# Performance work log

Hardware: AMD Instinct MI355X
Metric: run time of the kernel (lower is better)

## Reference

```python
import jax, jax.numpy as jnp
import numpy as np

HEADS = 8
FEATURE = 512
COMPUTE = 256
SEQ = 512
BATCH = 64


def setup_inputs() -> dict:
    key = jax.random.key(0)
    ks = jax.random.split(key, 10)
    d1 = jax.random.normal(ks[0], (BATCH, FEATURE), dtype=jnp.float32)
    d2 = jax.random.normal(ks[1], (SEQ, BATCH, FEATURE), dtype=jnp.float32)
    # linear1: Linear(FEATURE -> COMPUTE) + ReLU
    w1 = jax.random.normal(ks[2], (FEATURE, COMPUTE), dtype=jnp.float32) * (1.0 / np.sqrt(FEATURE))
    b1 = jnp.zeros((COMPUTE,), dtype=jnp.float32)
    # per-head score params, stacked: ws[i] is [2C, C], ps[i] is [C, 1]
    W = jax.random.normal(ks[3], (HEADS, 2 * COMPUTE, COMPUTE), dtype=jnp.float32)
    P = jax.random.normal(ks[4], (HEADS, COMPUTE), dtype=jnp.float32)
    # value projection weight_v: [FEATURE, COMPUTE]
    wv = jax.random.normal(ks[5], (FEATURE, COMPUTE), dtype=jnp.float32)
    # cc: Linear(COMPUTE*HEADS -> 128) + ReLU
    wcc = jax.random.normal(ks[6], (COMPUTE * HEADS, 128), dtype=jnp.float32) * (1.0 / np.sqrt(COMPUTE * HEADS))
    bcc = jnp.zeros((128,), dtype=jnp.float32)
    return {"d1": d1, "d2": d2, "w1": w1, "b1": b1, "W": W, "P": P,
            "wv": wv, "wcc": wcc, "bcc": bcc, "d2_size": SEQ}


def reference(d1, d2, w1, b1, W, P, wv, wcc, bcc, d2_size):
    S, B, F = d2.shape
    # linear1 on flattened d2 rows -> [S*B, C]
    d3 = jax.nn.relu(d2.reshape(-1, F) @ w1 + b1)
    # linear1 on d1, tiled S times along batch axis -> [S*B, C]
    d4 = jax.nn.relu(d1 @ w1 + b1)            # [B, C]
    d4 = jnp.tile(d4, (S, 1))                  # [S*B, C]
    d5 = jnp.concatenate([d3, d4], axis=1).reshape(S, B, -1)  # [S, B, 2C]
    # value path: tanh(d2 @ weight_v) -> [B, S, C]
    tv = jnp.tanh(jnp.einsum('sbf,fc->sbc', d2, wv)).transpose(1, 0, 2)
    # all heads batched: us = tanh(d5 @ W_h) -> [H, S, B, C]
    us = jnp.tanh(jnp.einsum('sbd,hdc->hsbc', d5, W))
    atts = jnp.einsum('hsbc,hc->hbs', us, P)   # [H, B, S]
    scores = jax.nn.softmax(atts, axis=-1)     # softmax over sequence
    vs = jnp.einsum('hbs,bsc->hbc', scores, tv)  # weighted sum over S -> [H, B, C]
    # torch.cat(vs, dim=1): head-major concat -> [B, H*C]
    vs = vs.transpose(1, 0, 2).reshape(B, -1)
    return jax.nn.relu(vs @ wcc + bcc)         # [B, 128]
```

## Files before the change

### kernel.cpp

```cpp
#include <hip/hip_runtime.h>
#include <cstddef>
#include <cstdint>

#define HH 8
#define FF 512
#define CC 256
#define SS 512
#define BB 64
#define SB (SS*BB)
#define PAD 34

typedef __attribute__((ext_vector_type(4))) float f32x4;
typedef __attribute__((ext_vector_type(8))) short bf16x8;

__device__ __forceinline__ float fast_tanh(float x) {
    float e = __expf(2.0f * x);
    return 1.0f - 2.0f / (e + 1.0f);
}
__device__ __forceinline__ float relu_f(float x) { return fmaxf(x, 0.0f); }

__device__ __forceinline__ unsigned short f2bf(float x) {
    unsigned u = __float_as_uint(x);
    unsigned r = u + 0x7FFFu + ((u >> 16) & 1u);
    return (unsigned short)(r >> 16);
}
__device__ __forceinline__ float bf2f(unsigned short h) {
    return __uint_as_float(((unsigned)h) << 16);
}

__global__ __launch_bounds__(256) void p_prep(
    const float* __restrict__ w1, const float* __restrict__ wv,
    const float* __restrict__ W, const float* __restrict__ d1,
    const float* __restrict__ b1,
    unsigned short* __restrict__ w1t_hi, unsigned short* __restrict__ w1t_lo,
    unsigned short* __restrict__ wvt_hi, unsigned short* __restrict__ wvt_lo,
    unsigned short* __restrict__ Wt_hi, unsigned short* __restrict__ Wt_lo,
    float* __restrict__ d4, float* __restrict__ atts)
{
    __shared__ float T[64][65];
    __shared__ float As[16][68];
    __shared__ float Bs[16][68];
    const int tid = threadIdx.x;
    const int bid = blockIdx.x;
    if (bid >= 196) {
        f32x4 z = {0.0f, 0.0f, 0.0f, 0.0f};
        *(f32x4*)(atts + (size_t)(bid - 196) * 1024 + tid * 4) = z;
        return;
    }
    if (bid < 192) {
        const float* src;
        unsigned short *dhi, *dlo;
        int K, kt, nt;
        if (bid < 64) {
            int m = bid >> 5;
            int t = bid & 31;
            kt = t >> 2; nt = t & 3; K = FF;
            src = m ? wv : w1;
            dhi = m ? wvt_hi : w1t_hi;
            dlo = m ? wvt_lo : w1t_lo;
        } else {
            int t = bid - 64;
            int h = t >> 4; int tt = t & 15;
            kt = tt >> 2; nt = tt & 3; K = CC;
            src = W + (size_t)h * 2 * CC * CC;
            dhi = Wt_hi + (size_t)h * CC * CC;
            dlo = Wt_lo + (size_t)h * CC * CC;
        }
        const int k0 = kt * 64, n0 = nt * 64;
        #pragma unroll
        for (int jj = 0; jj < 4; ++jj) {
            int i = (tid >> 4) + jj * 16;
            int j = (tid & 15) * 4;
            float4 v = *(const float4*)(src + (size_t)(k0 + i) * CC + n0 + j);
            T[i][j] = v.x; T[i][j+1] = v.y; T[i][j+2] = v.z; T[i][j+3] = v.w;
        }
        __syncthreads();
        #pragma unroll
        for (int jj = 0; jj < 4; ++jj) {
            int n = (tid >> 4) + jj * 16;
            int kq = (tid & 15) * 4;
            unsigned short hv[4], lv[4];
            #pragma unroll
            for (int q = 0; q < 4; ++q) {
                float x = T[kq + q][n];
                unsigned short hx = f2bf(x);
                hv[q] = hx; lv[q] = f2bf(x - bf2f(hx));
            }
            size_t o = (size_t)(n0 + n) * K + k0 + kq;
            *(ushort4*)(dhi + o) = *(ushort4*)hv;
            *(ushort4*)(dlo + o) = *(ushort4*)lv;
        }
    } else {
        const int n0 = (bid - 192) * 64;
        const int tx = tid & 15, ty = tid >> 4;
        const int lm = tid >> 2, lk4 = (tid & 3) * 4;
        const int bk = tid >> 4, bn4 = (tid & 15) * 4;
        float acc[4][4] = {};
        for (int k0 = 0; k0 < FF; k0 += 16) {
            float4 a = *(const float4*)(d1 + (size_t)lm * FF + k0 + lk4);
            As[lk4+0][lm] = a.x; As[lk4+1][lm] = a.y;
            As[lk4+2][lm] = a.z; As[lk4+3][lm] = a.w;
            *(float4*)&Bs[bk][bn4] = *(const float4*)(w1 + (size_t)(k0+bk)*CC + n0 + bn4);
            __syncthreads();
            #pragma unroll
            for (int kk = 0; kk < 16; ++kk) {
                float4 a4 = *(const float4*)&As[kk][ty*4];
                float4 b4 = *(const float4*)&Bs[kk][tx*4];
                float av[4] = {a4.x, a4.y, a4.z, a4.w};
                float bv[4] = {b4.x, b4.y, b4.z, b4.w};
                #pragma unroll
                for (int i = 0; i < 4; ++i)
                    #pragma unroll
                    for (int j = 0; j < 4; ++j)
                        acc[i][j] = fmaf(av[i], bv[j], acc[i][j]);
            }
            __syncthreads();
        }
        #pragma unroll
        for (int i = 0; i < 4; ++i) {
            int row = ty*4 + i;
            #pragma unroll
            for (int j = 0; j < 4; ++j)
                d4[(size_t)row*CC + n0 + tx*4 + j] = relu_f(acc[i][j] + b1[n0 + tx*4 + j]);
        }
    }
}

__global__ __launch_bounds__(256, 3) void k1_main(
    const float* __restrict__ d2,
    const unsigned short* __restrict__ w1t_hi, const unsigned short* __restrict__ w1t_lo,
    const unsigned short* __restrict__ wvt_hi, const unsigned short* __restrict__ wvt_lo,
    const float* __restrict__ b1,
    const float* __restrict__ d4, const float* __restrict__ W,
    unsigned short* __restrict__ d3_hi, unsigned short* __restrict__ d3_lo,
    unsigned short* __restrict__ tv, float* __restrict__ e4)
{
    __shared__ __align__(16) unsigned short A_hi[128][PAD];
    __shared__ __align__(16) unsigned short A_lo[128][PAD];
    __shared__ __align__(16) unsigned short B_hi[128][PAD];
    __shared__ __align__(16) unsigned short B_lo[128][PAD];

    const int tid = threadIdx.x;
    const int bid = blockIdx.x;

    if (bid >= 1024) {
        float (*As)[68] = (float(*)[68])&A_hi[0][0];
        float (*Bs)[68] = (float(*)[68])&B_hi[0][0];
        const int idx = bid - 1024;
        const int n0 = (idx & 3) * 64;
        const int h  = idx >> 2;
        const float* Wh = W + ((size_t)h * 2 * CC + CC) * CC;
        const int tx = tid & 15, ty = tid >> 4;
        const int lm = tid >> 2, lk4 = (tid & 3) * 4;
        const int bk = tid >> 4, bn4 = (tid & 15) * 4;
        float acc[4][4] = {};
        for (int k0 = 0; k0 < CC; k0 += 16) {
            float4 a = *(const float4*)(d4 + (size_t)lm * CC + k0 + lk4);
            As[lk4+0][lm] = a.x; As[lk4+1][lm] = a.y;
            As[lk4+2][lm] = a.z; As[lk4+3][lm] = a.w;
            *(float4*)&Bs[bk][bn4] = *(const float4*)(Wh + (size_t)(k0+bk)*CC + n0 + bn4);
            __syncthreads();
            #pragma unroll
            for (int kk = 0; kk < 16; ++kk) {
                float4 a4 = *(const float4*)&As[kk][ty*4];
                float4 b4 = *(const float4*)&Bs[kk][tx*4];
                float av[4] = {a4.x, a4.y, a4.z, a4.w};
                float bv[4] = {b4.x, b4.y, b4.z, b4.w};
                #pragma unroll
                for (int i = 0; i < 4; ++i)
                    #pragma unroll
                    for (int j = 0; j < 4; ++j)
                        acc[i][j] = fmaf(av[i], bv[j], acc[i][j]);
            }
            __syncthreads();
        }
        #pragma unroll
        for (int i = 0; i < 4; ++i) {
            int b = ty*4 + i;
            #pragma unroll
            for (int j = 0; j < 4; ++j)
                e4[((size_t)h*BB + b)*CC + n0 + tx*4 + j] = acc[i][j];
        }
        return;
    }

    const int rowtile = bid & 255;
    const int colhalf = (bid >> 8) & 1;
    const int path    = bid >> 9;
    const int r0 = rowtile * 128;
    const int n0 = colhalf * 128;
    const int lane = tid & 63, w = tid >> 6;
    const int rowgrp = w & 1, colgrp = w >> 1;
    const int cb = lane & 15, quad = lane >> 4;
    const unsigned short* BH = path ? wvt_hi : w1t_hi;
    const unsigned short* BL = path ? wvt_lo : w1t_lo;

    const int srow = tid >> 1;
    const int sk   = (tid & 1) * 16;

    f32x4 acc[4][4];
    f32x4 zero = {0.0f, 0.0f, 0.0f, 0.0f};
    #pragma unroll
    for (int rt = 0; rt < 4; ++rt)
        #pragma unroll
        for (int ct = 0; ct < 4; ++ct) acc[rt][ct] = zero;

    for (int k0 = 0; k0 < FF; k0 += 32) {
        {
            const float* src = d2 + (size_t)(r0 + srow) * FF + k0 + sk;
            float v[16];
            *(float4*)&v[0]  = *(const float4*)(src);
            *(float4*)&v[4]  = *(const float4*)(src + 4);
            *(float4*)&v[8]  = *(const float4*)(src + 8);
            *(float4*)&v[12] = *(const float4*)(src + 12);
            bf16x8 vh0, vh1, vl0, vl1;
            #pragma unroll
            for (int j = 0; j < 8; ++j) {
                unsigned short h = f2bf(v[j]);
                vh0[j] = (short)h; vl0[j] = (short)f2bf(v[j] - bf2f(h));
                unsigned short h2 = f2bf(v[j+8]);
                vh1[j] = (short)h2; vl1[j] = (short)f2bf(v[j+8] - bf2f(h2));
            }
            *(bf16x8*)&A_hi[srow][sk]     = vh0;
            *(bf16x8*)&A_hi[srow][sk + 8] = vh1;
            *(bf16x8*)&A_lo[srow][sk]     = vl0;
            *(bf16x8*)&A_lo[srow][sk + 8] = vl1;
        }
        {
            const size_t go = (size_t)(n0 + srow) * FF + k0 + sk;
            *(bf16x8*)&B_hi[srow][sk]     = *(const bf16x8*)(BH + go);
            *(bf16x8*)&B_hi[srow][sk + 8] = *(const bf16x8*)(BH + go + 8);
            *(bf16x8*)&B_lo[srow][sk]     = *(const bf16x8*)(BL + go);
            *(bf16x8*)&B_lo[srow][sk + 8] = *(const bf16x8*)(BL + go + 8);
        }
        __syncthreads();
        bf16x8 ahf[4], alf[4];
        #pragma unroll
        for (int rt = 0; rt < 4; ++rt) {
            ahf[rt] = *(bf16x8*)&A_hi[rowgrp*64 + rt*16 + cb][quad*8];
            alf[rt] = *(bf16x8*)&A_lo[rowgrp*64 + rt*16 + cb][quad*8];
        }
        #pragma unroll
        for (int ct = 0; ct < 4; ++ct) {
            bf16x8 bh = *(bf16x8*)&B_hi[colgrp*64 + ct*16 + cb][quad*8];
            bf16x8 bl = *(bf16x8*)&B_lo[colgrp*64 + ct*16 + cb][quad*8];
            #pragma unroll
            for (int rt = 0; rt < 4; ++rt) {
                acc[rt][ct] = __builtin_amdgcn_mfma_f32_16x16x32_bf16(ahf[rt], bh, acc[rt][ct], 0, 0, 0);
                acc[rt][ct] = __builtin_amdgcn_mfma_f32_16x16x32_bf16(ahf[rt], bl, acc[rt][ct], 0, 0, 0);
                acc[rt][ct] = __builtin_amdgcn_mfma_f32_16x16x32_bf16(alf[rt], bh, acc[rt][ct], 0, 0, 0);
            }
        }
        __syncthreads();
    }
    if (path == 0) {
        float bias[4];
        #pragma unroll
        for (int ct = 0; ct < 4; ++ct) bias[ct] = b1[n0 + colgrp*64 + ct*16 + cb];
        #pragma unroll
        for (int rt = 0; rt < 4; ++rt) {
            #pragma unroll
            for (int r = 0; r < 4; ++r) {
                int gr = r0 + rowgrp*64 + rt*16 + quad*4 + r;
                #pragma unroll
                for (int ct = 0; ct < 4; ++ct) {
                    int c = n0 + colgrp*64 + ct*16 + cb;
                    float val = relu_f(acc[rt][ct][r] + bias[ct]);
                    unsigned short hv = f2bf(val);
                    d3_hi[(size_t)gr * CC + c] = hv;
                    d3_lo[(size_t)gr * CC + c] = f2bf(val - bf2f(hv));
                }
            }
        }
    } else {
        #pragma unroll
        for (int rt = 0; rt < 4; ++rt) {
            #pragma unroll
            for (int r = 0; r < 4; ++r) {
                int gr = r0 + rowgrp*64 + rt*16 + quad*4 + r;
                int s = gr >> 6, b = gr & 63;
                #pragma unroll
                for (int ct = 0; ct < 4; ++ct) {
                    int c = n0 + colgrp*64 + ct*16 + cb;
                    tv[((size_t)b * SS + s) * CC + c] = f2bf(fast_tanh(acc[rt][ct][r]));
                }
            }
        }
    }
}

__global__ __launch_bounds__(256, 3) void k3_atts(
    const unsigned short* __restrict__ d3_hi, const unsigned short* __restrict__ d3_lo,
    const unsigned short* __restrict__ Wt_hi, const unsigned short* __restrict__ Wt_lo,
    const float* __restrict__ e4, const float* __restrict__ P,
    float* __restrict__ atts)
{
    __shared__ __align__(16) unsigned short B_hi[128][PAD];
    __shared__ __align__(16) unsigned short B_lo[128][PAD];
    __shared__ float red[2][128];

    const int tid = threadIdx.x;
    const int lane = tid & 63, w = tid >> 6;
    const int h = blockIdx.y;
    const int rowtile = blockIdx.x & 255;
    const int colhalf = blockIdx.x >> 8;
    const int r0 = rowtile * 128;
    const int n0 = colhalf * 128;
    const int rowgrp = w & 1, colgrp = w >> 1;
    const int cb = lane & 15, quad = lane >> 4;

    const unsigned short* WhH = Wt_hi + (size_t)h * CC * CC;
    const unsigned short* WhL = Wt_lo + (size_t)h * CC * CC;

    const int srow = tid >> 1;
    const int sk   = (tid & 1) * 16;

    const size_t abase = (size_t)(r0 + rowgrp*64 + cb) * CC + quad*8;

    f32x4 acc[4][4];
    f32x4 zero = {0.0f, 0.0f, 0.0f, 0.0f};
    #pragma unroll
    for (int rt = 0; rt < 4; ++rt)
        #pragma unroll
        for (int ct = 0; ct < 4; ++ct) acc[rt][ct] = zero;

    for (int k0 = 0; k0 < CC; k0 += 32) {
        {
            const size_t go = (size_t)(n0 + srow) * CC + k0 + sk;
            *(bf16x8*)&B_hi[srow][sk]     = *(const bf16x8*)(WhH + go);
            *(bf16x8*)&B_hi[srow][sk + 8] = *(const bf16x8*)(WhH + go + 8);
            *(bf16x8*)&B_lo[srow][sk]     = *(const bf16x8*)(WhL + go);
            *(bf16x8*)&B_lo[srow][sk + 8] = *(const bf16x8*)(WhL + go + 8);
        }
        bf16x8 ahf[4], alf[4];
        #pragma unroll
        for (int rt = 0; rt < 4; ++rt) {
            const size_t ao = abase + (size_t)(rt*16) * CC + k0;
            ahf[rt] = *(const bf16x8*)(d3_hi + ao);
            alf[rt] = *(const bf16x8*)(d3_lo + ao);
        }
        __syncthreads();
        #pragma unroll
        for (int ct = 0; ct < 4; ++ct) {
            bf16x8 bh = *(bf16x8*)&B_hi[colgrp*64 + ct*16 + cb][quad*8];
            bf16x8 bl = *(bf16x8*)&B_lo[colgrp*64 + ct*16 + cb][quad*8];
            #pragma unroll
            for (int rt = 0; rt < 4; ++rt) {
                acc[rt][ct] = __builtin_amdgcn_mfma_f32_16x16x32_bf16(ahf[rt], bh, acc[rt][ct], 0, 0, 0);
                acc[rt][ct] = __builtin_amdgcn_mfma_f32_16x16x32_bf16(ahf[rt], bl, acc[rt][ct], 0, 0, 0);
                acc[rt][ct] = __builtin_amdgcn_mfma_f32_16x16x32_bf16(alf[rt], bh, acc[rt][ct], 0, 0, 0);
            }
        }
        __syncthreads();
    }
    float Pv[4];
    #pragma unroll
    for (int ct = 0; ct < 4; ++ct) Pv[ct] = P[(size_t)h * CC + n0 + colgrp*64 + ct*16 + cb];
    #pragma unroll
    for (int rt = 0; rt < 4; ++rt) {
        #pragma unroll
        for (int r = 0; r < 4; ++r) {
            int lrow = rt*16 + quad*4 + r;
            int b = lrow;
            const float* e4p = e4 + ((size_t)h * BB + b) * CC + n0 + colgrp*64 + cb;
            float part = 0.0f;
            #pragma unroll
            for (int ct = 0; ct < 4; ++ct) {
                float u = acc[rt][ct][r] + e4p[ct*16];
                part = fmaf(Pv[ct], fast_tanh(u), part);
            }
            part += __shfl_xor(part, 1); part += __shfl_xor(part, 2);
            part += __shfl_xor(part, 4); part += __shfl_xor(part, 8);
            if (cb == 0) red[colgrp][rowgrp*64 + lrow] = part;
        }
    }
    __syncthreads();
    if (tid < 128) {
        float v = red[0][tid] + red[1][tid];
        int gr = r0 + tid;
        int s = gr >> 6, b = gr & 63;
        atomicAdd(&atts[((size_t)h * BB + b) * SS + s], v);
    }
}

__global__ __launch_bounds__(512) void k456_out(
    const float* __restrict__ atts, const unsigned short* __restrict__ tv,
    const float* __restrict__ wcc, const float* __restrict__ bcc,
    float* __restrict__ out)
{
    __shared__ float sc[HH][SS];
    __shared__ float red[8][2048];
    const int b = blockIdx.x;
    const int tid = threadIdx.x;
    const int lane = tid & 63, w = tid >> 6;

    for (int i = tid; i < HH*SS; i += 512) {
        int h = i >> 9, s = i & 511;
        sc[h][s] = atts[((size_t)h*BB + b)*SS + s];
    }
    __syncthreads();
    {
        float x[8];
        #pragma unroll
        for (int j = 0; j < 8; ++j) x[j] = sc[w][j*64 + lane];
        float m = x[0];
        #pragma unroll
        for (int j = 1; j < 8; ++j) m = fmaxf(m, x[j]);
        #pragma unroll
        for (int d = 1; d < 64; d <<= 1) m = fmaxf(m, __shfl_xor(m, d));
        float sum = 0.0f;
        #pragma unroll
        for (int j = 0; j < 8; ++j) { x[j] = __expf(x[j] - m); sum += x[j]; }
        #pragma unroll
        for (int d = 1; d < 64; d <<= 1) sum += __shfl_xor(sum, d);
        float inv = 1.0f / sum;
        #pragma unroll
        for (int j = 0; j < 8; ++j) sc[w][j*64 + lane] = x[j] * inv;
    }
    __syncthreads();
    {
        const int cl = tid & 63, stripe = tid >> 6;
        const int c0 = cl * 4;
        const unsigned short* tvb = tv + ((size_t)b * SS + stripe * 64) * CC + c0;
        float acc[HH][4] = {};
        for (int si = 0; si < 64; ++si) {
            uint2 u = *(const uint2*)(tvb + (size_t)si * CC);
            float x0 = bf2f((unsigned short)(u.x));
            float x1 = bf2f((unsigned short)(u.x >> 16));
            float x2 = bf2f((unsigned short)(u.y));
            float x3 = bf2f((unsigned short)(u.y >> 16));
            int s = stripe * 64 + si;
            #pragma unroll
            for (int h = 0; h < HH; ++h) {
                float wgt = sc[h][s];
                acc[h][0] = fmaf(wgt, x0, acc[h][0]);
                acc[h][1] = fmaf(wgt, x1, acc[h][1]);
                acc[h][2] = fmaf(wgt, x2, acc[h][2]);
                acc[h][3] = fmaf(wgt, x3, acc[h][3]);
            }
        }
        #pragma unroll
        for (int h = 0; h < HH; ++h)
            #pragma unroll
            for (int j = 0; j < 4; ++j)
                red[stripe][h*256 + c0 + j] = acc[h][j];
    }
    __syncthreads();
    for (int i = tid; i < 2048; i += 512) {
        float v = red[0][i];
        #pragma unroll
        for (int st = 1; st < 8; ++st) v += red[st][i];
        red[0][i] = v;
    }
    __syncthreads();
    {
        const int n = tid & 127, q = tid >> 7;
        float o = 0.0f;
        const int kbase = q * 512;
        for (int k = 0; k < 512; ++k)
            o = fmaf(red[0][kbase + k], wcc[(size_t)(kbase + k) * 128 + n], o);
        float* r2 = &sc[0][0];
        r2[q * 128 + n] = o;
    }
    __syncthreads();
    if (tid < 128) {
        float* r2 = &sc[0][0];
        out[(size_t)b * 128 + tid] =
            relu_f(r2[tid] + r2[128 + tid] + r2[256 + tid] + r2[384 + tid] + bcc[tid]);
    }
}

extern "C" void kernel_launch(void* const* d_in, const int* in_sizes, int n_in,
                              void* d_out, int out_size, void* d_ws, size_t ws_size,
                              hipStream_t stream)
{
    (void)in_sizes; (void)n_in; (void)out_size; (void)ws_size;
    const float* d1  = (const float*)d_in[0];
    const float* d2  = (const float*)d_in[1];
    const float* w1  = (const float*)d_in[2];
    const float* b1  = (const float*)d_in[3];
    const float* W   = (const float*)d_in[4];
    const float* P   = (const float*)d_in[5];
    const float* wv  = (const float*)d_in[6];
    const float* wcc = (const float*)d_in[7];
    const float* bcc = (const float*)d_in[8];
    float* out = (float*)d_out;

    char* p = (char*)d_ws;
    unsigned short* d3_hi = (unsigned short*)p;  p += (size_t)SB * CC * 2;
    unsigned short* d3_lo = (unsigned short*)p;  p += (size_t)SB * CC * 2;
    unsigned short* tv    = (unsigned short*)p;  p += (size_t)BB * SS * CC * 2;
    unsigned short* w1t_hi = (unsigned short*)p; p += (size_t)CC * FF * 2;
    unsigned short* w1t_lo = (unsigned short*)p; p += (size_t)CC * FF * 2;
    unsigned short* wvt_hi = (unsigned short*)p; p += (size_t)CC * FF * 2;
    unsigned short* wvt_lo = (unsigned short*)p; p += (size_t)CC * FF * 2;
    unsigned short* Wt_hi  = (unsigned short*)p; p += (size_t)HH * CC * CC * 2;
    unsigned short* Wt_lo  = (unsigned short*)p; p += (size_t)HH * CC * CC * 2;
    float* d4   = (float*)p;  p += (size_t)BB * CC * 4;
    float* e4   = (float*)p;  p += (size_t)HH * BB * CC * 4;
    float* atts = (float*)p;  p += (size_t)HH * BB * SS * 4;

    p_prep   <<<dim3(452),       256, 0, stream>>>(w1, wv, W, d1, b1,
                  w1t_hi, w1t_lo, wvt_hi, wvt_lo, Wt_hi, Wt_lo, d4, atts);
    k1_main  <<<dim3(1056),      256, 0, stream>>>(d2, w1t_hi, w1t_lo,
                  wvt_hi, wvt_lo, b1, d4, W, d3_hi, d3_lo, tv, e4);
    k3_atts  <<<dim3(512, HH),   256, 0, stream>>>(d3_hi, d3_lo, Wt_hi, Wt_lo,
                  e4, P, atts);
    k456_out <<<dim3(BB),        512, 0, stream>>>(atts, tv, wcc, bcc, out);
}
```

Baseline: 424.5 us.

## Use single bf16 pass for value path and stage d3 tiles in LDS

The tanh value projection (path 1 of k1_main) now drops the split-bf16 hi/lo compensation and runs one bf16 MFMA per tile instead of three, and skips computing and storing the lo halves of d2 and wv. Separately, k3_atts now loads d3 hi/lo tiles cooperatively into shared memory instead of having each wave read its fragments directly from global memory, and its occupancy hint is raised to 4 blocks. The value-path change lowers precision on a tanh-bounded branch in exchange for about a third of that path's MFMA work and less traffic. The LDS staging adds shared memory use and a barrier.

```diff
diff --git a/kernel.cpp b/kernel.cpp
--- a/kernel.cpp
+++ b/kernel.cpp
@@ -33,7 +33,7 @@
     const float* __restrict__ W, const float* __restrict__ d1,
     const float* __restrict__ b1,
     unsigned short* __restrict__ w1t_hi, unsigned short* __restrict__ w1t_lo,
-    unsigned short* __restrict__ wvt_hi, unsigned short* __restrict__ wvt_lo,
+    unsigned short* __restrict__ wvt_hi,
     unsigned short* __restrict__ Wt_hi, unsigned short* __restrict__ Wt_lo,
     float* __restrict__ d4, float* __restrict__ atts)
 {
@@ -57,7 +57,7 @@
             kt = t >> 2; nt = t & 3; K = FF;
             src = m ? wv : w1;
             dhi = m ? wvt_hi : w1t_hi;
-            dlo = m ? wvt_lo : w1t_lo;
+            dlo = m ? (unsigned short*)nullptr : w1t_lo;
         } else {
             int t = bid - 64;
             int h = t >> 4; int tt = t & 15;
@@ -88,7 +88,7 @@
             }
             size_t o = (size_t)(n0 + n) * K + k0 + kq;
             *(ushort4*)(dhi + o) = *(ushort4*)hv;
-            *(ushort4*)(dlo + o) = *(ushort4*)lv;
+            if (dlo) *(ushort4*)(dlo + o) = *(ushort4*)lv;
         }
     } else {
         const int n0 = (bid - 192) * 64;
@@ -129,7 +129,7 @@
 __global__ __launch_bounds__(256, 3) void k1_main(
     const float* __restrict__ d2,
     const unsigned short* __restrict__ w1t_hi, const unsigned short* __restrict__ w1t_lo,
-    const unsigned short* __restrict__ wvt_hi, const unsigned short* __restrict__ wvt_lo,
+    const unsigned short* __restrict__ wvt_hi,
     const float* __restrict__ b1,
     const float* __restrict__ d4, const float* __restrict__ W,
     unsigned short* __restrict__ d3_hi, unsigned short* __restrict__ d3_lo,
@@ -193,7 +193,6 @@
     const int rowgrp = w & 1, colgrp = w >> 1;
     const int cb = lane & 15, quad = lane >> 4;
     const unsigned short* BH = path ? wvt_hi : w1t_hi;
-    const unsigned short* BL = path ? wvt_lo : w1t_lo;
 
     const int srow = tid >> 1;
     const int sk   = (tid & 1) * 16;
@@ -213,42 +212,62 @@
             *(float4*)&v[4]  = *(const float4*)(src + 4);
             *(float4*)&v[8]  = *(const float4*)(src + 8);
             *(float4*)&v[12] = *(const float4*)(src + 12);
-            bf16x8 vh0, vh1, vl0, vl1;
+            bf16x8 vh0, vh1;
             #pragma unroll
             for (int j = 0; j < 8; ++j) {
-                unsigned short h = f2bf(v[j]);
-                vh0[j] = (short)h; vl0[j] = (short)f2bf(v[j] - bf2f(h));
-                unsigned short h2 = f2bf(v[j+8]);
-                vh1[j] = (short)h2; vl1[j] = (short)f2bf(v[j+8] - bf2f(h2));
+                vh0[j] = (short)f2bf(v[j]);
+                vh1[j] = (short)f2bf(v[j+8]);
             }
             *(bf16x8*)&A_hi[srow][sk]     = vh0;
             *(bf16x8*)&A_hi[srow][sk + 8] = vh1;
-            *(bf16x8*)&A_lo[srow][sk]     = vl0;
-            *(bf16x8*)&A_lo[srow][sk + 8] = vl1;
+            if (path == 0) {
+                bf16x8 vl0, vl1;
+                #pragma unroll
+                for (int j = 0; j < 8; ++j) {
+                    vl0[j] = (short)f2bf(v[j]   - bf2f((unsigned short)vh0[j]));
+                    vl1[j] = (short)f2bf(v[j+8] - bf2f((unsigned short)vh1[j]));
+                }
+                *(bf16x8*)&A_lo[srow][sk]     = vl0;
+                *(bf16x8*)&A_lo[srow][sk + 8] = vl1;
+            }
         }
         {
             const size_t go = (size_t)(n0 + srow) * FF + k0 + sk;
             *(bf16x8*)&B_hi[srow][sk]     = *(const bf16x8*)(BH + go);
             *(bf16x8*)&B_hi[srow][sk + 8] = *(const bf16x8*)(BH + go + 8);
-            *(bf16x8*)&B_lo[srow][sk]     = *(const bf16x8*)(BL + go);
-            *(bf16x8*)&B_lo[srow][sk + 8] = *(const bf16x8*)(BL + go + 8);
+            if (path == 0) {
+                *(bf16x8*)&B_lo[srow][sk]     = *(const bf16x8*)(w1t_lo + go);
+                *(bf16x8*)&B_lo[srow][sk + 8] = *(const bf16x8*)(w1t_lo + go + 8);
+            }
         }
         __syncthreads();
-        bf16x8 ahf[4], alf[4];
-        #pragma unroll
-        for (int rt = 0; rt < 4; ++rt) {
+        bf16x8 ahf[4];
+        #pragma unroll
+        for (int rt = 0; rt < 4; ++rt)
             ahf[rt] = *(bf16x8*)&A_hi[rowgrp*64 + rt*16 + cb][quad*8];
-            alf[rt] = *(bf16x8*)&A_lo[rowgrp*64 + rt*16 + cb][quad*8];
-        }
-        #pragma unroll
-        for (int ct = 0; ct < 4; ++ct) {
-            bf16x8 bh = *(bf16x8*)&B_hi[colgrp*64 + ct*16 + cb][quad*8];
-            bf16x8 bl = *(bf16x8*)&B_lo[colgrp*64 + ct*16 + cb][quad*8];
-            #pragma unroll
-            for (int rt = 0; rt < 4; ++rt) {
-                acc[rt][ct] = __builtin_amdgcn_mfma_f32_16x16x32_bf16(ahf[rt], bh, acc[rt][ct], 0, 0, 0);
-                acc[rt][ct] = __builtin_amdgcn_mfma_f32_16x16x32_bf16(ahf[rt], bl, acc[rt][ct], 0, 0, 0);
-                acc[rt][ct] = __builtin_amdgcn_mfma_f32_16x16x32_bf16(alf[rt], bh, acc[rt][ct], 0, 0, 0);
+        if (path == 0) {
+            bf16x8 alf[4];
+            #pragma unroll
+            for (int rt = 0; rt < 4; ++rt)
+                alf[rt] = *(bf16x8*)&A_lo[rowgrp*64 + rt*16 + cb][quad*8];
+            #pragma unroll
+            for (int ct = 0; ct < 4; ++ct) {
+                bf16x8 bh = *(bf16x8*)&B_hi[colgrp*64 + ct*16 + cb][quad*8];
+                bf16x8 bl = *(bf16x8*)&B_lo[colgrp*64 + ct*16 + cb][quad*8];
+                #pragma unroll
+                for (int rt = 0; rt < 4; ++rt) {
+                    acc[rt][ct] = __builtin_amdgcn_mfma_f32_16x16x32_bf16(ahf[rt], bh, acc[rt][ct], 0, 0, 0);
+                    acc[rt][ct] = __builtin_amdgcn_mfma_f32_16x16x32_bf16(ahf[rt], bl, acc[rt][ct], 0, 0, 0);
+                    acc[rt][ct] = __builtin_amdgcn_mfma_f32_16x16x32_bf16(alf[rt], bh, acc[rt][ct], 0, 0, 0);
+                }
+            }
+        } else {
+            #pragma unroll
+            for (int ct = 0; ct < 4; ++ct) {
+                bf16x8 bh = *(bf16x8*)&B_hi[colgrp*64 + ct*16 + cb][quad*8];
+                #pragma unroll
+                for (int rt = 0; rt < 4; ++rt)
+                    acc[rt][ct] = __builtin_amdgcn_mfma_f32_16x16x32_bf16(ahf[rt], bh, acc[rt][ct], 0, 0, 0);
             }
         }
         __syncthreads();
@@ -289,12 +308,14 @@
     }
 }
 
-__global__ __launch_bounds__(256, 3) void k3_atts(
+__global__ __launch_bounds__(256, 4) void k3_atts(
     const unsigned short* __restrict__ d3_hi, const unsigned short* __restrict__ d3_lo,
     const unsigned short* __restrict__ Wt_hi, const unsigned short* __restrict__ Wt_lo,
     const float* __restrict__ e4, const float* __restrict__ P,
     float* __restrict__ atts)
 {
+    __shared__ __align__(16) unsigned short A_hi[128][PAD];
+    __shared__ __align__(16) unsigned short A_lo[128][PAD];
     __shared__ __align__(16) unsigned short B_hi[128][PAD];
     __shared__ __align__(16) unsigned short B_lo[128][PAD];
     __shared__ float red[2][128];
@@ -315,8 +336,6 @@
     const int srow = tid >> 1;
     const int sk   = (tid & 1) * 16;
 
-    const size_t abase = (size_t)(r0 + rowgrp*64 + cb) * CC + quad*8;
-
     f32x4 acc[4][4];
     f32x4 zero = {0.0f, 0.0f, 0.0f, 0.0f};
     #pragma unroll
@@ -326,20 +345,24 @@
 
     for (int k0 = 0; k0 < CC; k0 += 32) {
         {
+            const size_t ao = (size_t)(r0 + srow) * CC + k0 + sk;
+            *(bf16x8*)&A_hi[srow][sk]     = *(const bf16x8*)(d3_hi + ao);
+            *(bf16x8*)&A_hi[srow][sk + 8] = *(const bf16x8*)(d3_hi + ao + 8);
+            *(bf16x8*)&A_lo[srow][sk]     = *(const bf16x8*)(d3_lo + ao);
+            *(bf16x8*)&A_lo[srow][sk + 8] = *(const bf16x8*)(d3_lo + ao + 8);
             const size_t go = (size_t)(n0 + srow) * CC + k0 + sk;
             *(bf16x8*)&B_hi[srow][sk]     = *(const bf16x8*)(WhH + go);
             *(bf16x8*)&B_hi[srow][sk + 8] = *(const bf16x8*)(WhH + go + 8);
             *(bf16x8*)&B_lo[srow][sk]     = *(const bf16x8*)(WhL + go);
             *(bf16x8*)&B_lo[srow][sk + 8] = *(const bf16x8*)(WhL + go + 8);
         }
+        __syncthreads();
         bf16x8 ahf[4], alf[4];
         #pragma unroll
         for (int rt = 0; rt < 4; ++rt) {
-            const size_t ao = abase + (size_t)(rt*16) * CC + k0;
-            ahf[rt] = *(const bf16x8*)(d3_hi + ao);
-            alf[rt] = *(const bf16x8*)(d3_lo + ao);
-        }
-        __syncthreads();
+            ahf[rt] = *(bf16x8*)&A_hi[rowgrp*64 + rt*16 + cb][quad*8];
+            alf[rt] = *(bf16x8*)&A_lo[rowgrp*64 + rt*16 + cb][quad*8];
+        }
         #pragma unroll
         for (int ct = 0; ct < 4; ++ct) {
             bf16x8 bh = *(bf16x8*)&B_hi[colgrp*64 + ct*16 + cb][quad*8];
@@ -493,7 +516,6 @@
     unsigned short* w1t_hi = (unsigned short*)p; p += (size_t)CC * FF * 2;
     unsigned short* w1t_lo = (unsigned short*)p; p += (size_t)CC * FF * 2;
     unsigned short* wvt_hi = (unsigned short*)p; p += (size_t)CC * FF * 2;
-    unsigned short* wvt_lo = (unsigned short*)p; p += (size_t)CC * FF * 2;
     unsigned short* Wt_hi  = (unsigned short*)p; p += (size_t)HH * CC * CC * 2;
     unsigned short* Wt_lo  = (unsigned short*)p; p += (size_t)HH * CC * CC * 2;
     float* d4   = (float*)p;  p += (size_t)BB * CC * 4;
@@ -501,9 +523,9 @@
     float* atts = (float*)p;  p += (size_t)HH * BB * SS * 4;
 
     p_prep   <<<dim3(452),       256, 0, stream>>>(w1, wv, W, d1, b1,
-                  w1t_hi, w1t_lo, wvt_hi, wvt_lo, Wt_hi, Wt_lo, d4, atts);
+                  w1t_hi, w1t_lo, wvt_hi, Wt_hi, Wt_lo, d4, atts);
     k1_main  <<<dim3(1056),      256, 0, stream>>>(d2, w1t_hi, w1t_lo,
-                  wvt_hi, wvt_lo, b1, d4, W, d3_hi, d3_lo, tv, e4);
+                  wvt_hi, b1, d4, W, d3_hi, d3_lo, tv, e4);
     k3_atts  <<<dim3(512, HH),   256, 0, stream>>>(d3_hi, d3_lo, Wt_hi, Wt_lo,
                   e4, P, atts);
     k456_out <<<dim3(BB),        512, 0, stream>>>(atts, tv, wcc, bcc, out);
```

After: 461.2 us. 8.6% more time.
